# Optimization experiments

Hardware: AMD Instinct MI355X
Metric: run time of the kernel (lower is better)

The kernel has to match this reference:

```python
import jax, jax.numpy as jnp
import numpy as np

B, L, D = 4, 1024, 1024
H, DK, DV = 16, 64, 64
HID = 4 * D
EPS = 1e-5


def layer_norm(x, w, b):
    m = x.mean(-1, keepdims=True)
    v = ((x - m) ** 2).mean(-1, keepdims=True)
    return (x - m) * jax.lax.rsqrt(v + EPS) * w + b


def sln(hl, w, ln_w, ln_b, gamma, beta):
    # Self-modulated LayerNorm: gamma * w * LN(hl) + beta * w
    return gamma * w * layer_norm(hl, ln_w, ln_b) + beta * w


def setup_inputs() -> dict:
    key = jax.random.key(0)
    ks = jax.random.split(key, 20)
    s = 0.02
    inp = {
        "q": jax.random.normal(ks[0], (B, L, D), jnp.float32),
        "k": jax.random.normal(ks[1], (B, L, D), jnp.float32),
        "v": jax.random.normal(ks[2], (B, L, D), jnp.float32),
        "z": jax.random.normal(ks[3], (B, L, D), jnp.float32),
        # projections stored [in, out] (torch Linear applies x @ W.T + b)
        "wq_w": jax.random.normal(ks[4], (D, H * DK), jnp.float32) * s,
        "wq_b": jnp.zeros((H * DK,), jnp.float32),
        "wk_w": jax.random.normal(ks[5], (D, H * DK), jnp.float32) * s,
        "wk_b": jnp.zeros((H * DK,), jnp.float32),
        "wv_w": jax.random.normal(ks[6], (D, H * DV), jnp.float32) * s,
        "wv_b": jnp.zeros((H * DV,), jnp.float32),
        "fc_w": jax.random.normal(ks[7], (H * DV, D), jnp.float32) * s,
        "fc_b": jnp.zeros((D,), jnp.float32),
        "mlp1_w": jax.random.normal(ks[8], (D, HID), jnp.float32) * s,
        "mlp1_b": jnp.zeros((HID,), jnp.float32),
        "mlp2_w": jax.random.normal(ks[9], (HID, D), jnp.float32) * s,
        "mlp2_b": jnp.zeros((D,), jnp.float32),
        "ln1_w": jnp.ones((D,), jnp.float32),
        "ln1_b": jnp.zeros((D,), jnp.float32),
        "g1": jax.random.normal(ks[10], (1, 1, 1), jnp.float32),
        "b1": jax.random.normal(ks[11], (1, 1, 1), jnp.float32),
        "ln2_w": jnp.ones((D,), jnp.float32),
        "ln2_b": jnp.zeros((D,), jnp.float32),
        "g2": jax.random.normal(ks[12], (1, 1, 1), jnp.float32),
        "b2": jax.random.normal(ks[13], (1, 1, 1), jnp.float32),
    }
    return inp


def reference(q, k, v, z,
              wq_w, wq_b, wk_w, wk_b, wv_w, wv_b, fc_w, fc_b,
              mlp1_w, mlp1_b, mlp2_w, mlp2_b,
              ln1_w, ln1_b, g1, b1, ln2_w, ln2_b, g2, b2):
    scale = 1.0 / np.sqrt(DK).astype(np.float32)
    q = sln(q, z, ln1_w, ln1_b, g1, b1)
    residual = q
    qh = (q @ wq_w + wq_b).reshape(B, L, H, DK)
    kh = (k @ wk_w + wk_b).reshape(B, L, H, DK)
    vh = (v @ wv_w + wv_b).reshape(B, L, H, DV)
    # scores per (head, batch) matching torch layout (n_head*sz_b, Lq, Lk)
    attn = jnp.einsum("bqhd,bkhd->hbqk", qh, kh) * scale
    attn = jax.nn.softmax(attn, axis=-1)
    out = jnp.einsum("hbqk,bkhd->bqhd", attn, vh).reshape(B, L, H * DV)
    out = out @ fc_w + fc_b
    out = out + residual
    h = sln(out, z, ln2_w, ln2_b, g2, b2)
    h = jax.nn.gelu(h @ mlp1_w + mlp1_b, approximate=False)
    out = (h @ mlp2_w + mlp2_b) + out
    return out, attn.reshape(H * B, L, L)
```

## Files before the change

### kernel.cpp

```cpp
#include <hip/hip_runtime.h>
#include <math.h>

namespace {

constexpr int kL  = 1024;
constexpr int kD  = 1024;
constexpr int kB  = 4;
constexpr int kH  = 16;
constexpr int kDK = 64;
constexpr int kHID = 4096;

typedef unsigned short ushort_t;
typedef short  s16x8 __attribute__((ext_vector_type(8)));
typedef float  f32x4 __attribute__((ext_vector_type(4)));
typedef unsigned short u16x4 __attribute__((ext_vector_type(4)));

__device__ __forceinline__ ushort_t f2bf(float f) {
    unsigned u = __float_as_uint(f);
    unsigned r = u + 0x7fffu + ((u >> 16) & 1u);
    return (ushort_t)(r >> 16);
}

__device__ __forceinline__ void gld16(const void* g, void* l) {
    __builtin_amdgcn_global_load_lds((__attribute__((address_space(1))) void*)(g),
                                     (__attribute__((address_space(3))) void*)(l),
                                     16, 0, 0);
}

__device__ __forceinline__ float wred_sum(float v) {
    #pragma unroll
    for (int o = 32; o > 0; o >>= 1) v += __shfl_xor(v, o, 64);
    return v;
}

__global__ __launch_bounds__(256) void sln_kernel(
    const float* __restrict__ x, const float* __restrict__ z,
    const float* __restrict__ lnw, const float* __restrict__ lnb,
    const float* __restrict__ g, const float* __restrict__ bt,
    float* __restrict__ outf, ushort_t* __restrict__ outb)
{
    const int row = blockIdx.x;
    const int tid = threadIdx.x;
    const size_t base = (size_t)row * kD;
    float4 xv = ((const float4*)(x + base))[tid];
    float s  = xv.x + xv.y + xv.z + xv.w;
    float sq = xv.x * xv.x + xv.y * xv.y + xv.z * xv.z + xv.w * xv.w;
    __shared__ float r1[4], r2[4];
    float ws = wred_sum(s), wq = wred_sum(sq);
    int lane = tid & 63, wid = tid >> 6;
    if (lane == 0) { r1[wid] = ws; r2[wid] = wq; }
    __syncthreads();
    float st = r1[0] + r1[1] + r1[2] + r1[3];
    float qt = r2[0] + r2[1] + r2[2] + r2[3];
    float mean = st * (1.0f / kD);
    float var  = qt * (1.0f / kD) - mean * mean;
    float rs = rsqrtf(var + 1e-5f);
    float gv = g[0], bv = bt[0];
    float4 zv = ((const float4*)(z + base))[tid];
    float4 wv = ((const float4*)lnw)[tid];
    float4 lb = ((const float4*)lnb)[tid];
    float4 o;
    o.x = zv.x * (gv * ((xv.x - mean) * rs * wv.x + lb.x) + bv);
    o.y = zv.y * (gv * ((xv.y - mean) * rs * wv.y + lb.y) + bv);
    o.z = zv.z * (gv * ((xv.z - mean) * rs * wv.z + lb.z) + bv);
    o.w = zv.w * (gv * ((xv.w - mean) * rs * wv.w + lb.w) + bv);
    if (outf) ((float4*)(outf + base))[tid] = o;
    u16x4 ob; ob[0] = f2bf(o.x); ob[1] = f2bf(o.y); ob[2] = f2bf(o.z); ob[3] = f2bf(o.w);
    ((u16x4*)(outb + base))[tid] = ob;
}

__global__ __launch_bounds__(256) void cvt_bf16(
    const float* __restrict__ x, ushort_t* __restrict__ y)
{
    int i = blockIdx.x * 256 + threadIdx.x;
    f32x4 v = ((const f32x4*)x)[i];
    u16x4 o; o[0] = f2bf(v[0]); o[1] = f2bf(v[1]); o[2] = f2bf(v[2]); o[3] = f2bf(v[3]);
    ((u16x4*)y)[i] = o;
}

__global__ __launch_bounds__(256) void twcvt(
    const float* __restrict__ src, ushort_t* __restrict__ dst, int R, int C)
{
    __shared__ float t[32][33];
    int c0 = blockIdx.x * 32, r0 = blockIdx.y * 32;
    int tx = threadIdx.x & 31, ty = threadIdx.x >> 5;
    #pragma unroll
    for (int i = 0; i < 4; i++) {
        int r = ty + i * 8;
        t[r][tx] = src[(size_t)(r0 + r) * C + c0 + tx];
    }
    __syncthreads();
    #pragma unroll
    for (int i = 0; i < 4; i++) {
        int c = ty + i * 8;
        dst[(size_t)(c0 + c) * R + r0 + tx] = f2bf(t[tx][c]);
    }
}

__global__ __launch_bounds__(256) void vtrans(
    const ushort_t* __restrict__ vh, ushort_t* __restrict__ vhT)
{
    __shared__ ushort_t t[32][33];
    int p = blockIdx.z, b = p & 3, h = p >> 2;
    int j0 = blockIdx.x * 32, d0 = blockIdx.y * 32;
    int tx = threadIdx.x & 31, ty = threadIdx.x >> 5;
    const ushort_t* src = vh + (size_t)b * (kL * kD) + h * kDK;
    #pragma unroll
    for (int i = 0; i < 4; i++) {
        int j = ty + i * 8;
        t[j][tx] = src[(size_t)(j0 + j) * kD + d0 + tx];
    }
    __syncthreads();
    ushort_t* dst = vhT + (size_t)p * (kDK * kL);
    #pragma unroll
    for (int i = 0; i < 4; i++) {
        int d = ty + i * 8;
        dst[(size_t)(d0 + d) * kL + j0 + tx] = t[tx][d];
    }
}

__global__ __launch_bounds__(256) void mgemm(
    const ushort_t* __restrict__ A, int lda,
    const ushort_t* __restrict__ Bt, int ldb,
    void* __restrict__ Cv, int ldc, int K,
    const float* __restrict__ bias, const float* __restrict__ res,
    float scale, int flags, int mode,
    const float* __restrict__ bias1, const float* __restrict__ bias2)
{
    __shared__ __align__(16) ushort_t As[128 * 32];
    __shared__ __align__(16) ushort_t Bs[128 * 32];
    float*    Cf = (float*)Cv;
    ushort_t* Cb = (ushort_t*)Cv;
    if (mode == 2) {
        int z = blockIdx.z;
        A  += (size_t)z * (4096u * 1024u);
        Bt += (size_t)z * (1024u * 1024u);
        Cb += (size_t)z * (4096u * 1024u);
        if (z == 1) bias = bias1;
        else if (z == 2) bias = bias2;
    }
    const int tid = threadIdx.x;
    const int lane = tid & 63, w = tid >> 6;
    const int m0 = blockIdx.y * 128, n0 = blockIdx.x * 128;
    const int r0 = tid >> 2;
    const int c0 = (tid & 3) ^ (r0 & 3);
    const ushort_t* Ag0 = A  + (size_t)(m0 + r0) * lda + c0 * 8;
    const ushort_t* Ag1 = Ag0 + (size_t)64 * lda;
    const ushort_t* Bg0 = Bt + (size_t)(n0 + r0) * ldb + c0 * 8;
    const ushort_t* Bg1 = Bg0 + (size_t)64 * ldb;
    char* AsW = (char*)As + w * 1024;
    char* BsW = (char*)Bs + w * 1024;
    const int wm = (w & 1) * 64, wn = (w >> 1) * 64;
    const int fn = lane & 15, q = lane >> 4;
    int aoff[4], boff[4];
    #pragma unroll
    for (int i = 0; i < 4; i++) {
        int ra = wm + i * 16 + fn;
        aoff[i] = (ra * 4 + (q ^ (ra & 3))) * 16;
        int rb = wn + i * 16 + fn;
        boff[i] = (rb * 4 + (q ^ (rb & 3))) * 16;
    }
    f32x4 acc[4][4] = {};
    for (int k0 = 0; k0 < K; k0 += 32) {
        gld16(Ag0 + k0, AsW);
        gld16(Ag1 + k0, AsW + 4096);
        gld16(Bg0 + k0, BsW);
        gld16(Bg1 + k0, BsW + 4096);
        __syncthreads();
        s16x8 af[4], bfr[4];
        #pragma unroll
        for (int i = 0; i < 4; i++) {
            af[i]  = *(const s16x8*)((const char*)As + aoff[i]);
            bfr[i] = *(const s16x8*)((const char*)Bs + boff[i]);
        }
        #pragma unroll
        for (int mi = 0; mi < 4; mi++)
            #pragma unroll
            for (int ni = 0; ni < 4; ni++)
                acc[mi][ni] = __builtin_amdgcn_mfma_f32_16x16x32_bf16(
                    af[mi], bfr[ni], acc[mi][ni], 0, 0, 0);
        __syncthreads();
    }
    #pragma unroll
    for (int mi = 0; mi < 4; mi++) {
        #pragma unroll
        for (int ni = 0; ni < 4; ni++) {
            #pragma unroll
            for (int r = 0; r < 4; r++) {
                int gm = m0 + wm + mi * 16 + q * 4 + r;
                int gn = n0 + wn + ni * 16 + fn;
                float v = acc[mi][ni][r] * scale;
                if (bias) v += bias[gn];
                if (flags & 1) v = 0.5f * v * (1.0f + erff(v * 0.70710678118654752f));
                if (res) v += res[(size_t)gm * ldc + gn];
                if (flags & 2) Cb[(size_t)gm * ldc + gn] = f2bf(v);
                else           Cf[(size_t)gm * ldc + gn] = v;
            }
        }
    }
}

__global__ __launch_bounds__(512) void fused_attn(
    const ushort_t* __restrict__ qh, const ushort_t* __restrict__ kh,
    const ushort_t* __restrict__ vhT, float* __restrict__ attn,
    ushort_t* __restrict__ ctx)
{
    __shared__ __align__(16) char PlBuf[8 * 4096];
    __shared__ float redm[8][32];
    __shared__ float reds[8][32];
    const int orig = blockIdx.y * 32 + blockIdx.x;
    const int nf = (orig & 7) * 256 + (orig >> 3);
    const int p = nf >> 5, b = p & 3, h = p >> 2;
    const int m0 = (nf & 31) * 32;
    const int tid = threadIdx.x;
    const int lane = tid & 63, w = tid >> 6;
    const int fn = lane & 15, q = lane >> 4;
    const ushort_t* Qb = qh + (size_t)b * (kL * kD) + h * 64;
    const ushort_t* Kb = kh + (size_t)b * (kL * kD) + h * 64;
    float* Pp = attn + (size_t)p * kL * kL;

    f32x4 acc[2][8] = {};
    #pragma unroll
    for (int kk = 0; kk < 2; kk++) {
        s16x8 aq[2], bq[8];
        #pragma unroll
        for (int mi = 0; mi < 2; mi++)
            aq[mi] = *(const s16x8*)(Qb + (size_t)(m0 + mi * 16 + fn) * kD + kk * 32 + q * 8);
        #pragma unroll
        for (int ni = 0; ni < 8; ni++)
            bq[ni] = *(const s16x8*)(Kb + (size_t)(w * 128 + ni * 16 + fn) * kD + kk * 32 + q * 8);
        #pragma unroll
        for (int mi = 0; mi < 2; mi++)
            #pragma unroll
            for (int ni = 0; ni < 8; ni++)
                acc[mi][ni] = __builtin_amdgcn_mfma_f32_16x16x32_bf16(
                    aq[mi], bq[ni], acc[mi][ni], 0, 0, 0);
    }

    float mloc[2][4];
    #pragma unroll
    for (int mi = 0; mi < 2; mi++) {
        #pragma unroll
        for (int r = 0; r < 4; r++) {
            float m = -3.0e38f;
            #pragma unroll
            for (int ni = 0; ni < 8; ni++) {
                acc[mi][ni][r] *= 0.125f;
                m = fmaxf(m, acc[mi][ni][r]);
            }
            mloc[mi][r] = m;
        }
    }
    #pragma unroll
    for (int o = 1; o < 16; o <<= 1) {
        #pragma unroll
        for (int mi = 0; mi < 2; mi++)
            #pragma unroll
            for (int r = 0; r < 4; r++)
                mloc[mi][r] = fmaxf(mloc[mi][r], __shfl_xor(mloc[mi][r], o, 64));
    }
    if (fn == 0) {
        #pragma unroll
        for (int mi = 0; mi < 2; mi++)
            #pragma unroll
            for (int r = 0; r < 4; r++)
                redm[w][mi * 16 + q * 4 + r] = mloc[mi][r];
    }
    __syncthreads();
    #pragma unroll
    for (int mi = 0; mi < 2; mi++) {
        #pragma unroll
        for (int r = 0; r < 4; r++) {
            int row = mi * 16 + q * 4 + r;
            float m = redm[0][row];
            #pragma unroll
            for (int w2 = 1; w2 < 8; w2++) m = fmaxf(m, redm[w2][row]);
            float s = 0.f;
            #pragma unroll
            for (int ni = 0; ni < 8; ni++) {
                float e = __expf(acc[mi][ni][r] - m);
                acc[mi][ni][r] = e;
                s += e;
            }
            mloc[mi][r] = s;
        }
    }
    #pragma unroll
    for (int o = 1; o < 16; o <<= 1) {
        #pragma unroll
        for (int mi = 0; mi < 2; mi++)
            #pragma unroll
            for (int r = 0; r < 4; r++)
                mloc[mi][r] += __shfl_xor(mloc[mi][r], o, 64);
    }
    if (fn == 0) {
        #pragma unroll
        for (int mi = 0; mi < 2; mi++)
            #pragma unroll
            for (int r = 0; r < 4; r++)
                reds[w][mi * 16 + q * 4 + r] = mloc[mi][r];
    }
    __syncthreads();
    float inv[2][4];
    #pragma unroll
    for (int mi = 0; mi < 2; mi++) {
        #pragma unroll
        for (int r = 0; r < 4; r++) {
            int row = mi * 16 + q * 4 + r;
            float s = reds[0][row];
            #pragma unroll
            for (int w2 = 1; w2 < 8; w2++) s += reds[w2][row];
            inv[mi][r] = 1.0f / s;
        }
    }
    #pragma unroll
    for (int mi = 0; mi < 2; mi++)
        #pragma unroll
        for (int ni = 0; ni < 8; ni++)
            #pragma unroll
            for (int r = 0; r < 4; r++)
                __builtin_nontemporal_store(
                    acc[mi][ni][r] * inv[mi][r],
                    &Pp[(size_t)(m0 + mi * 16 + q * 4 + r) * kL + w * 128 + ni * 16 + fn]);

    const ushort_t* Vb = vhT + (size_t)p * (kDK * kL);
    char* Plw = PlBuf + w * 4096;
    f32x4 acc2[2][4] = {};
    #pragma unroll
    for (int half = 0; half < 2; half++) {
        #pragma unroll
        for (int mi = 0; mi < 2; mi++)
            #pragma unroll
            for (int ni = 0; ni < 4; ni++)
                #pragma unroll
                for (int r = 0; r < 4; r++) {
                    int row = mi * 16 + q * 4 + r;
                    int cl  = ni * 16 + fn;
                    *(ushort_t*)(Plw + ((row * 128 + cl * 2) ^ ((row & 7) << 4)))
                        = f2bf(acc[mi][half * 4 + ni][r]);
                }
        #pragma unroll
        for (int kh = 0; kh < 2; kh++) {
            int kk = half * 2 + kh;
            s16x8 pa[2];
            #pragma unroll
            for (int mi = 0; mi < 2; mi++) {
                int row = mi * 16 + fn;
                pa[mi] = *(const s16x8*)(Plw +
                    ((row * 128 + (kh * 32 + q * 8) * 2) ^ ((row & 7) << 4)));
            }
            #pragma unroll
            for (int nj = 0; nj < 4; nj++) {
                s16x8 bv = *(const s16x8*)(Vb + (size_t)(nj * 16 + fn) * kL +
                                           w * 128 + kk * 32 + q * 8);
                #pragma unroll
                for (int mi = 0; mi < 2; mi++)
                    acc2[mi][nj] = __builtin_amdgcn_mfma_f32_16x16x32_bf16(
                        pa[mi], bv, acc2[mi][nj], 0, 0, 0);
            }
        }
    }
    #pragma unroll
    for (int mi = 0; mi < 2; mi++)
        #pragma unroll
        for (int nj = 0; nj < 4; nj++)
            #pragma unroll
            for (int r = 0; r < 4; r++)
                acc2[mi][nj][r] *= inv[mi][r];

    __syncthreads();
    float (*cred)[2048] = (float (*)[2048])PlBuf;
    if (w < 4) {
        #pragma unroll
        for (int mi = 0; mi < 2; mi++)
            #pragma unroll
            for (int nj = 0; nj < 4; nj++)
                #pragma unroll
                for (int r = 0; r < 4; r++)
                    cred[w][(mi * 16 + q * 4 + r) * 64 + nj * 16 + fn] = acc2[mi][nj][r];
    }
    __syncthreads();
    if (w >= 4) {
        #pragma unroll
        for (int mi = 0; mi < 2; mi++)
            #pragma unroll
            for (int nj = 0; nj < 4; nj++)
                #pragma unroll
                for (int r = 0; r < 4; r++)
                    cred[w - 4][(mi * 16 + q * 4 + r) * 64 + nj * 16 + fn] += acc2[mi][nj][r];
    }
    __syncthreads();
    {
        int idx0 = tid * 4;
        int row = idx0 >> 6, d0 = idx0 & 63;
        f32x4 s0 = *(const f32x4*)&cred[0][idx0];
        #pragma unroll
        for (int wb = 1; wb < 4; wb++) {
            f32x4 t = *(const f32x4*)&cred[wb][idx0];
            s0[0] += t[0]; s0[1] += t[1]; s0[2] += t[2]; s0[3] += t[3];
        }
        u16x4 o;
        o[0] = f2bf(s0[0]); o[1] = f2bf(s0[1]); o[2] = f2bf(s0[2]); o[3] = f2bf(s0[3]);
        *(u16x4*)(ctx + (size_t)b * (kL * kD) + (size_t)(m0 + row) * kD + h * 64 + d0) = o;
    }
}

}

extern "C" void kernel_launch(void* const* d_in, const int* in_sizes, int n_in,
                              void* d_out, int out_size, void* d_ws, size_t ws_size,
                              hipStream_t stream)
{
    (void)in_sizes; (void)n_in; (void)out_size; (void)ws_size;
    const float* q      = (const float*)d_in[0];
    const float* k      = (const float*)d_in[1];
    const float* v      = (const float*)d_in[2];
    const float* z      = (const float*)d_in[3];
    const float* wq_w   = (const float*)d_in[4];
    const float* wq_b   = (const float*)d_in[5];
    const float* wk_w   = (const float*)d_in[6];
    const float* wk_b   = (const float*)d_in[7];
    const float* wv_w   = (const float*)d_in[8];
    const float* wv_b   = (const float*)d_in[9];
    const float* fc_w   = (const float*)d_in[10];
    const float* fc_b   = (const float*)d_in[11];
    const float* mlp1_w = (const float*)d_in[12];
    const float* mlp1_b = (const float*)d_in[13];
    const float* mlp2_w = (const float*)d_in[14];
    const float* mlp2_b = (const float*)d_in[15];
    const float* ln1_w  = (const float*)d_in[16];
    const float* ln1_b  = (const float*)d_in[17];
    const float* g1     = (const float*)d_in[18];
    const float* b1     = (const float*)d_in[19];
    const float* ln2_w  = (const float*)d_in[20];
    const float* ln2_b  = (const float*)d_in[21];
    const float* g2     = (const float*)d_in[22];
    const float* b2     = (const float*)d_in[23];

    float* out0 = (float*)d_out;
    float* attn = (float*)d_out + (size_t)kB * kL * kD;

    char* arena = (char*)d_ws;
    const size_t MB = 1u << 20;
    float*    qp   = (float*)(arena);
    ushort_t* qh   = (ushort_t*)(arena + 16 * MB);
    ushort_t* kh   = (ushort_t*)(arena + 24 * MB);
    ushort_t* vh   = (ushort_t*)(arena + 32 * MB);
    ushort_t* vhT  = (ushort_t*)(arena + 40 * MB);
    ushort_t* hid  = (ushort_t*)(arena + 16 * MB);
    ushort_t* qb   = (ushort_t*)(arena + 48 * MB);
    ushort_t* kb   = (ushort_t*)(arena + 56 * MB);
    float*    out1 = (float*)(arena + 48 * MB);
    ushort_t* vb   = (ushort_t*)(arena + 64 * MB);
    ushort_t* ctx  = (ushort_t*)(arena + 64 * MB);
    ushort_t* h2   = (ushort_t*)(arena + 72 * MB);
    ushort_t* wqT  = (ushort_t*)(arena + 80 * MB);
    ushort_t* wkT  = (ushort_t*)(arena + 82 * MB);
    ushort_t* wvT  = (ushort_t*)(arena + 84 * MB);
    ushort_t* fcT  = (ushort_t*)(arena + 86 * MB);
    ushort_t* m1T  = (ushort_t*)(arena + 88 * MB);
    ushort_t* m2T  = (ushort_t*)(arena + 96 * MB);

    dim3 blk(256);
    twcvt<<<dim3(32, 32), blk, 0, stream>>>(wq_w, wqT, kD, kH * kDK);
    twcvt<<<dim3(32, 32), blk, 0, stream>>>(wk_w, wkT, kD, kH * kDK);
    twcvt<<<dim3(32, 32), blk, 0, stream>>>(wv_w, wvT, kD, kH * kDK);
    twcvt<<<dim3(32, 32), blk, 0, stream>>>(fc_w, fcT, kH * kDK, kD);
    twcvt<<<dim3(128, 32), blk, 0, stream>>>(mlp1_w, m1T, kD, kHID);
    twcvt<<<dim3(32, 128), blk, 0, stream>>>(mlp2_w, m2T, kHID, kD);
    cvt_bf16<<<dim3(4096), blk, 0, stream>>>(k, kb);
    cvt_bf16<<<dim3(4096), blk, 0, stream>>>(v, vb);
    sln_kernel<<<dim3(kB * kL), blk, 0, stream>>>(q, z, ln1_w, ln1_b, g1, b1, qp, qb);
    mgemm<<<dim3(8, 32, 3), blk, 0, stream>>>(qb, kD, wqT, kD, qh, kD, kD,
                                              wq_b, nullptr, 1.0f, 2, 2, wk_b, wv_b);
    vtrans<<<dim3(32, 2, 64), blk, 0, stream>>>(vh, vhT);
    fused_attn<<<dim3(kL / 32, 64), dim3(512), 0, stream>>>(qh, kh, vhT, attn, ctx);
    mgemm<<<dim3(8, 32, 1), blk, 0, stream>>>(ctx, kD, fcT, kD, out1, kD, kD,
                                              fc_b, qp, 1.0f, 0, 0, nullptr, nullptr);
    sln_kernel<<<dim3(kB * kL), blk, 0, stream>>>(out1, z, ln2_w, ln2_b, g2, b2, nullptr, h2);
    mgemm<<<dim3(32, 32, 1), blk, 0, stream>>>(h2, kD, m1T, kD, hid, kHID, kD,
                                               mlp1_b, nullptr, 1.0f, 3, 0, nullptr, nullptr);
    mgemm<<<dim3(8, 32, 1), blk, 0, stream>>>(hid, kHID, m2T, kHID, out0, kD, kHID,
                                              mlp2_b, out1, 1.0f, 0, 0, nullptr, nullptr);
}
```

Before: 824.3 us.

## Split-K the narrow GEMMs, remap workgroups, and batch small conversion launches

The fc and mlp2 GEMMs (N=1024, 256 tiles) now run split-K with two K halves over grid z. The second half writes a float partial that is reduced either in the LN2 kernel (which now takes an extra addend and writes back the sum) or by a new add kernel. GEMM workgroups are also remapped with an 8-way interleave to change cache locality. The four weight transposes and the two k/v bf16 conversions are merged into single launches to cut launch count. The split-K path costs extra partial-buffer traffic and reduction kernels in exchange for more workgroups filling the CUs.

```diff
diff --git a/kernel.cpp b/kernel.cpp
--- a/kernel.cpp
+++ b/kernel.cpp
@@ -34,7 +34,8 @@
 }
 
 __global__ __launch_bounds__(256) void sln_kernel(
-    const float* __restrict__ x, const float* __restrict__ z,
+    const float* __restrict__ x, const float* __restrict__ x2, float* __restrict__ xw,
+    const float* __restrict__ z,
     const float* __restrict__ lnw, const float* __restrict__ lnb,
     const float* __restrict__ g, const float* __restrict__ bt,
     float* __restrict__ outf, ushort_t* __restrict__ outb)
@@ -43,6 +44,11 @@
     const int tid = threadIdx.x;
     const size_t base = (size_t)row * kD;
     float4 xv = ((const float4*)(x + base))[tid];
+    if (x2) {
+        float4 a = ((const float4*)(x2 + base))[tid];
+        xv.x += a.x; xv.y += a.y; xv.z += a.z; xv.w += a.w;
+    }
+    if (xw) ((float4*)(xw + base))[tid] = xv;
     float s  = xv.x + xv.y + xv.z + xv.w;
     float sq = xv.x * xv.x + xv.y * xv.y + xv.z * xv.z + xv.w * xv.w;
     __shared__ float r1[4], r2[4];
@@ -69,13 +75,27 @@
     ((u16x4*)(outb + base))[tid] = ob;
 }
 
-__global__ __launch_bounds__(256) void cvt_bf16(
-    const float* __restrict__ x, ushort_t* __restrict__ y)
+__global__ __launch_bounds__(256) void cvt2_bf16(
+    const float* __restrict__ kx, const float* __restrict__ vx, ushort_t* __restrict__ kv)
+{
+    int b = blockIdx.x;
+    bool isv = b >= 4096;
+    const float* src = isv ? vx : kx;
+    ushort_t* dst = kv + (isv ? (size_t)4194304 : 0);
+    int i = (b & 4095) * 256 + threadIdx.x;
+    f32x4 v = ((const f32x4*)src)[i];
+    u16x4 o; o[0] = f2bf(v[0]); o[1] = f2bf(v[1]); o[2] = f2bf(v[2]); o[3] = f2bf(v[3]);
+    ((u16x4*)dst)[i] = o;
+}
+
+__global__ __launch_bounds__(256) void addf4(
+    float* __restrict__ dst, const float* __restrict__ src)
 {
     int i = blockIdx.x * 256 + threadIdx.x;
-    f32x4 v = ((const f32x4*)x)[i];
-    u16x4 o; o[0] = f2bf(v[0]); o[1] = f2bf(v[1]); o[2] = f2bf(v[2]); o[3] = f2bf(v[3]);
-    ((u16x4*)y)[i] = o;
+    f32x4 d = ((const f32x4*)dst)[i];
+    f32x4 s = ((const f32x4*)src)[i];
+    d[0] += s[0]; d[1] += s[1]; d[2] += s[2]; d[3] += s[3];
+    ((f32x4*)dst)[i] = d;
 }
 
 __global__ __launch_bounds__(256) void twcvt(
@@ -94,6 +114,30 @@
     for (int i = 0; i < 4; i++) {
         int c = ty + i * 8;
         dst[(size_t)(c0 + c) * R + r0 + tx] = f2bf(t[tx][c]);
+    }
+}
+
+__global__ __launch_bounds__(256) void twcvt4(
+    const float* __restrict__ s0, const float* __restrict__ s1,
+    const float* __restrict__ s2, const float* __restrict__ s3,
+    ushort_t* __restrict__ dst)
+{
+    __shared__ float t[32][33];
+    int zz = blockIdx.z;
+    const float* src = zz == 0 ? s0 : zz == 1 ? s1 : zz == 2 ? s2 : s3;
+    ushort_t* d = dst + (size_t)zz * 1048576;
+    int c0 = blockIdx.x * 32, r0 = blockIdx.y * 32;
+    int tx = threadIdx.x & 31, ty = threadIdx.x >> 5;
+    #pragma unroll
+    for (int i = 0; i < 4; i++) {
+        int r = ty + i * 8;
+        t[r][tx] = src[(size_t)(r0 + r) * 1024 + c0 + tx];
+    }
+    __syncthreads();
+    #pragma unroll
+    for (int i = 0; i < 4; i++) {
+        int c = ty + i * 8;
+        d[(size_t)(c0 + c) * 1024 + r0 + tx] = f2bf(t[tx][c]);
     }
 }
 
@@ -125,23 +169,33 @@
     void* __restrict__ Cv, int ldc, int K,
     const float* __restrict__ bias, const float* __restrict__ res,
     float scale, int flags, int mode,
-    const float* __restrict__ bias1, const float* __restrict__ bias2)
+    const float* __restrict__ bias1, const float* __restrict__ bias2,
+    void* __restrict__ Cv2)
 {
     __shared__ __align__(16) ushort_t As[128 * 32];
     __shared__ __align__(16) ushort_t Bs[128 * 32];
-    float*    Cf = (float*)Cv;
-    ushort_t* Cb = (ushort_t*)Cv;
     if (mode == 2) {
         int z = blockIdx.z;
         A  += (size_t)z * (4096u * 1024u);
         Bt += (size_t)z * (1024u * 1024u);
-        Cb += (size_t)z * (4096u * 1024u);
+        Cv = (void*)((ushort_t*)Cv + (size_t)z * (4096u * 1024u));
         if (z == 1) bias = bias1;
         else if (z == 2) bias = bias2;
-    }
+    } else if (mode == 3) {
+        int z = blockIdx.z;
+        A  += (size_t)z * K;
+        Bt += (size_t)z * K;
+        if (z == 1) { Cv = Cv2; bias = nullptr; res = nullptr; flags = 0; }
+    }
+    float*    Cf = (float*)Cv;
+    ushort_t* Cb = (ushort_t*)Cv;
+    const int nx = gridDim.x, nwg = nx * gridDim.y;
+    int f = blockIdx.y * nx + blockIdx.x;
+    int rr = (f & 7) * (nwg >> 3) + (f >> 3);
+    const int bx = rr % nx, by = rr / nx;
     const int tid = threadIdx.x;
     const int lane = tid & 63, w = tid >> 6;
-    const int m0 = blockIdx.y * 128, n0 = blockIdx.x * 128;
+    const int m0 = by * 128, n0 = bx * 128;
     const int r0 = tid >> 2;
     const int c0 = (tid & 3) ^ (r0 & 3);
     const ushort_t* Ag0 = A  + (size_t)(m0 + r0) * lda + c0 * 8;
@@ -340,14 +394,14 @@
                         = f2bf(acc[mi][half * 4 + ni][r]);
                 }
         #pragma unroll
-        for (int kh = 0; kh < 2; kh++) {
-            int kk = half * 2 + kh;
+        for (int kh2 = 0; kh2 < 2; kh2++) {
+            int kk = half * 2 + kh2;
             s16x8 pa[2];
             #pragma unroll
             for (int mi = 0; mi < 2; mi++) {
                 int row = mi * 16 + fn;
                 pa[mi] = *(const s16x8*)(Plw +
-                    ((row * 128 + (kh * 32 + q * 8) * 2) ^ ((row & 7) << 4)));
+                    ((row * 128 + (kh2 * 32 + q * 8) * 2) ^ ((row & 7) << 4)));
             }
             #pragma unroll
             for (int nj = 0; nj < 4; nj++) {
@@ -443,43 +497,42 @@
     char* arena = (char*)d_ws;
     const size_t MB = 1u << 20;
     float*    qp   = (float*)(arena);
-    ushort_t* qh   = (ushort_t*)(arena + 16 * MB);
-    ushort_t* kh   = (ushort_t*)(arena + 24 * MB);
-    ushort_t* vh   = (ushort_t*)(arena + 32 * MB);
-    ushort_t* vhT  = (ushort_t*)(arena + 40 * MB);
-    ushort_t* hid  = (ushort_t*)(arena + 16 * MB);
-    ushort_t* qb   = (ushort_t*)(arena + 48 * MB);
-    ushort_t* kb   = (ushort_t*)(arena + 56 * MB);
-    float*    out1 = (float*)(arena + 48 * MB);
-    ushort_t* vb   = (ushort_t*)(arena + 64 * MB);
-    ushort_t* ctx  = (ushort_t*)(arena + 64 * MB);
-    ushort_t* h2   = (ushort_t*)(arena + 72 * MB);
+    ushort_t* qb   = (ushort_t*)(arena + 16 * MB);
+    ushort_t* kb   = (ushort_t*)(arena + 24 * MB);
+    ushort_t* vb   = (ushort_t*)(arena + 32 * MB);
+    ushort_t* qh   = (ushort_t*)(arena + 40 * MB);
+    ushort_t* kh   = (ushort_t*)(arena + 48 * MB);
+    ushort_t* vh   = (ushort_t*)(arena + 56 * MB);
+    ushort_t* vhT  = (ushort_t*)(arena + 32 * MB);
+    ushort_t* ctx  = (ushort_t*)(arena + 56 * MB);
+    float*    fcP  = (float*)(arena + 16 * MB);
+    ushort_t* h2   = (ushort_t*)(arena + 32 * MB);
+    float*    out1 = (float*)(arena + 64 * MB);
+    ushort_t* hid  = (ushort_t*)(arena);
+    float*    m2P  = (float*)(arena + 40 * MB);
     ushort_t* wqT  = (ushort_t*)(arena + 80 * MB);
-    ushort_t* wkT  = (ushort_t*)(arena + 82 * MB);
-    ushort_t* wvT  = (ushort_t*)(arena + 84 * MB);
     ushort_t* fcT  = (ushort_t*)(arena + 86 * MB);
     ushort_t* m1T  = (ushort_t*)(arena + 88 * MB);
     ushort_t* m2T  = (ushort_t*)(arena + 96 * MB);
 
     dim3 blk(256);
-    twcvt<<<dim3(32, 32), blk, 0, stream>>>(wq_w, wqT, kD, kH * kDK);
-    twcvt<<<dim3(32, 32), blk, 0, stream>>>(wk_w, wkT, kD, kH * kDK);
-    twcvt<<<dim3(32, 32), blk, 0, stream>>>(wv_w, wvT, kD, kH * kDK);
-    twcvt<<<dim3(32, 32), blk, 0, stream>>>(fc_w, fcT, kH * kDK, kD);
+    twcvt4<<<dim3(32, 32, 4), blk, 0, stream>>>(wq_w, wk_w, wv_w, fc_w, wqT);
     twcvt<<<dim3(128, 32), blk, 0, stream>>>(mlp1_w, m1T, kD, kHID);
     twcvt<<<dim3(32, 128), blk, 0, stream>>>(mlp2_w, m2T, kHID, kD);
-    cvt_bf16<<<dim3(4096), blk, 0, stream>>>(k, kb);
-    cvt_bf16<<<dim3(4096), blk, 0, stream>>>(v, vb);
-    sln_kernel<<<dim3(kB * kL), blk, 0, stream>>>(q, z, ln1_w, ln1_b, g1, b1, qp, qb);
+    cvt2_bf16<<<dim3(8192), blk, 0, stream>>>(k, v, kb);
+    sln_kernel<<<dim3(kB * kL), blk, 0, stream>>>(q, nullptr, nullptr, z,
+                                                  ln1_w, ln1_b, g1, b1, qp, qb);
     mgemm<<<dim3(8, 32, 3), blk, 0, stream>>>(qb, kD, wqT, kD, qh, kD, kD,
-                                              wq_b, nullptr, 1.0f, 2, 2, wk_b, wv_b);
+                                              wq_b, nullptr, 1.0f, 2, 2, wk_b, wv_b, nullptr);
     vtrans<<<dim3(32, 2, 64), blk, 0, stream>>>(vh, vhT);
     fused_attn<<<dim3(kL / 32, 64), dim3(512), 0, stream>>>(qh, kh, vhT, attn, ctx);
-    mgemm<<<dim3(8, 32, 1), blk, 0, stream>>>(ctx, kD, fcT, kD, out1, kD, kD,
-                                              fc_b, qp, 1.0f, 0, 0, nullptr, nullptr);
-    sln_kernel<<<dim3(kB * kL), blk, 0, stream>>>(out1, z, ln2_w, ln2_b, g2, b2, nullptr, h2);
+    mgemm<<<dim3(8, 32, 2), blk, 0, stream>>>(ctx, kD, fcT, kD, out1, kD, kD / 2,
+                                              fc_b, qp, 1.0f, 0, 3, nullptr, nullptr, fcP);
+    sln_kernel<<<dim3(kB * kL), blk, 0, stream>>>(out1, fcP, out1, z,
+                                                  ln2_w, ln2_b, g2, b2, nullptr, h2);
     mgemm<<<dim3(32, 32, 1), blk, 0, stream>>>(h2, kD, m1T, kD, hid, kHID, kD,
-                                               mlp1_b, nullptr, 1.0f, 3, 0, nullptr, nullptr);
-    mgemm<<<dim3(8, 32, 1), blk, 0, stream>>>(hid, kHID, m2T, kHID, out0, kD, kHID,
-                                              mlp2_b, out1, 1.0f, 0, 0, nullptr, nullptr);
-}
+                                               mlp1_b, nullptr, 1.0f, 3, 0, nullptr, nullptr, nullptr);
+    mgemm<<<dim3(8, 32, 2), blk, 0, stream>>>(hid, kHID, m2T, kHID, out0, kD, kHID / 2,
+                                              mlp2_b, out1, 1.0f, 0, 3, nullptr, nullptr, m2P);
+    addf4<<<dim3(4096), blk, 0, stream>>>(out0, m2P);
+}
```

After: 780.6 us. 5.3% less time.
